# Kernel tuning notes

Hardware: AMD Instinct MI355X
Metric: run time of the kernel (lower is better)

Reference implementation:

```python
import jax, jax.numpy as jnp
import numpy as np

N = 50000      # nodes
E = 800000     # edges (avg degree 16)
IN, H, OUT = 128, 256, 2
BN_EPS = 1e-5


def setup_inputs() -> dict:
    key = jax.random.key(0)
    ks = jax.random.split(key, 24)
    w = lambda k, s: jax.random.normal(k, s, jnp.float32) * 0.05
    inp = {
        "x": jax.random.normal(ks[0], (N, IN), jnp.float32),
        "edge_index": jax.random.randint(ks[1], (2, E), 0, N, jnp.int64),
    }
    # GINConv 1 MLP: Linear(IN,H) -> BN(H) -> ReLU -> Linear(H,H) -> ReLU
    inp.update(c1_W1=w(ks[2], (IN, H)), c1_b1=w(ks[3], (H,)),
               c1_g=jnp.ones((H,), jnp.float32), c1_be=jnp.zeros((H,), jnp.float32),
               c1_W2=w(ks[4], (H, H)), c1_b2=w(ks[5], (H,)))
    # GINConv 2
    inp.update(c2_W1=w(ks[6], (H, H)), c2_b1=w(ks[7], (H,)),
               c2_g=jnp.ones((H,), jnp.float32), c2_be=jnp.zeros((H,), jnp.float32),
               c2_W2=w(ks[8], (H, H)), c2_b2=w(ks[9], (H,)))
    # GINConv 3
    inp.update(c3_W1=w(ks[10], (H, H)), c3_b1=w(ks[11], (H,)),
               c3_g=jnp.ones((H,), jnp.float32), c3_be=jnp.zeros((H,), jnp.float32),
               c3_W2=w(ks[12], (H, H)), c3_b2=w(ks[13], (H,)))
    # readout head
    inp.update(lin1_W=w(ks[14], (3 * H, 3 * H)), lin1_b=w(ks[15], (3 * H,)),
               lin2_W=w(ks[16], (3 * H, OUT)), lin2_b=w(ks[17], (OUT,)))
    return inp


def _gin_conv(x, src, dst, W1, b1, g, be, W2, b2):
    # sum-aggregate neighbor features: agg[i] = sum_{e: dst[e]==i} x[src[e]]
    agg = jax.ops.segment_sum(x[src], dst, num_segments=N)
    h = (x + agg) @ W1 + b1            # (1+eps)*x + agg, eps=0
    mu = h.mean(axis=0)
    var = h.var(axis=0)                # biased var, as torch BN training
    h = jax.nn.relu((h - mu) * jax.lax.rsqrt(var + BN_EPS) * g + be)
    return jax.nn.relu(h @ W2 + b2)


def reference(x, edge_index,
              c1_W1, c1_b1, c1_g, c1_be, c1_W2, c1_b2,
              c2_W1, c2_b1, c2_g, c2_be, c2_W2, c2_b2,
              c3_W1, c3_b1, c3_g, c3_be, c3_W2, c3_b2,
              lin1_W, lin1_b, lin2_W, lin2_b):
    src, dst = edge_index[0], edge_index[1]
    h1 = _gin_conv(x, src, dst, c1_W1, c1_b1, c1_g, c1_be, c1_W2, c1_b2)
    h2 = _gin_conv(h1, src, dst, c2_W1, c2_b1, c2_g, c2_be, c2_W2, c2_b2)
    h3 = _gin_conv(h2, src, dst, c3_W1, c3_b1, c3_g, c3_be, c3_W2, c3_b2)
    h = jnp.concatenate((h1, h2, h3), axis=1)        # [N, 3H]
    h = jax.nn.relu(h @ lin1_W + lin1_b)
    h = h @ lin2_W + lin2_b                          # [N, OUT]
    return h, jax.nn.softmax(h, axis=1)
```

## Files before the change

kernel.cpp:

```cpp
#include <hip/hip_runtime.h>
#include <hip/hip_bf16.h>


#define GIN_N_FEAT_IN 128
#define GIN_H 256
#define M_PAD_ROWS 50176

typedef short short8 __attribute__((ext_vector_type(8)));
typedef float f32x4 __attribute__((ext_vector_type(4)));

__device__ inline ushort f32_to_bf16(float f) {
    union { float f; uint u; } x; x.f = f;
    uint r = x.u + 0x7fff + ((x.u >> 16) & 1);
    return (ushort)(r >> 16);
}
__device__ inline float bf16_to_f32(uint h) {
    union { uint u; float f; } x; x.u = h << 16;
    return x.f;
}
__device__ inline uint pack_bf16(float lo, float hi) {
    return (uint)f32_to_bf16(lo) | ((uint)f32_to_bf16(hi) << 16);
}

__device__ inline void gload_lds16(const ushort* g, ushort* l) {
    __builtin_amdgcn_global_load_lds(
        (const __attribute__((address_space(1))) void*)g,
        (__attribute__((address_space(3))) void*)l, 16, 0, 0);
}


__global__ void cvt_f32_bf16(const float* __restrict__ in, ushort* __restrict__ out, int npairs) {
    for (int i = blockIdx.x * blockDim.x + threadIdx.x; i < npairs; i += gridDim.x * blockDim.x) {
        float2 v = ((const float2*)in)[i];
        ((uint*)out)[i] = pack_bf16(v.x, v.y);
    }
}

struct WPrep {
    const float* src[7];
    ushort* dst[7];
    int R[7];
    int C[7];
};

__global__ void prep_weights(WPrep p) {
    int which = blockIdx.y;
    int R = p.R[which], C = p.C[which];
    int total = R * C;
    const float* src = p.src[which];
    ushort* dst = p.dst[which];
    for (int idx = blockIdx.x * blockDim.x + threadIdx.x; idx < total;
         idx += gridDim.x * blockDim.x) {
        int r = idx / C, c = idx - r * C;
        dst[(size_t)c * R + r] = f32_to_bf16(src[idx]);
    }
}


__global__ void count_kernel(const int* __restrict__ ei, int* __restrict__ deg, int E) {
    for (int e = blockIdx.x * blockDim.x + threadIdx.x; e < E; e += gridDim.x * blockDim.x) {
        atomicAdd(&deg[ei[E + e]], 1);
    }
}

__global__ void scan_chunk(const int* __restrict__ deg, int* __restrict__ row_start,
                           int* __restrict__ chunk_sums, int N) {
    __shared__ int sm[256];
    int tid = threadIdx.x;
    int idx = blockIdx.x * 256 + tid;
    int v = (idx < N) ? deg[idx] : 0;
    sm[tid] = v;
    __syncthreads();
    #pragma unroll
    for (int off = 1; off < 256; off <<= 1) {
        int t = (tid >= off) ? sm[tid - off] : 0;
        __syncthreads();
        sm[tid] += t;
        __syncthreads();
    }
    if (idx < N) row_start[idx] = sm[tid] - v;
    if (tid == 255) chunk_sums[blockIdx.x] = sm[255];
}

__global__ void scan_tops(int* __restrict__ chunk_sums, int* __restrict__ row_start,
                          int nchunks, int N, int E) {
    __shared__ int sm[256];
    int tid = threadIdx.x;
    int v = (tid < nchunks) ? chunk_sums[tid] : 0;
    sm[tid] = v;
    __syncthreads();
    #pragma unroll
    for (int off = 1; off < 256; off <<= 1) {
        int t = (tid >= off) ? sm[tid - off] : 0;
        __syncthreads();
        sm[tid] += t;
        __syncthreads();
    }
    if (tid < nchunks) chunk_sums[tid] = sm[tid] - v;
    if (tid == 0) row_start[N] = E;
}

__global__ void scan_add(int* __restrict__ row_start, int* __restrict__ cursor,
                         const int* __restrict__ chunk_sums, int N) {
    int idx = blockIdx.x * 256 + threadIdx.x;
    if (idx < N) {
        int v = row_start[idx] + chunk_sums[blockIdx.x];
        row_start[idx] = v;
        cursor[idx] = v;
    }
}

__global__ void scatter_kernel(const int* __restrict__ ei, int* __restrict__ cursor,
                               int* __restrict__ perm, int E) {
    for (int e = blockIdx.x * blockDim.x + threadIdx.x; e < E; e += gridDim.x * blockDim.x) {
        int d = ei[E + e];
        int pos = atomicAdd(&cursor[d], 1);
        perm[pos] = ei[e];
    }
}


template <int W>
__global__ void agg2(const ushort* __restrict__ xsrc, int stride,
                     const int* __restrict__ row_start, const int* __restrict__ perm,
                     ushort* __restrict__ out, int N) {
    constexpr int PL = W / 64;
    int node = blockIdx.x * 4 + (threadIdx.x >> 6);
    if (node >= N) return;
    const int lane = threadIdx.x & 63;
    const size_t loff = (size_t)lane * PL;

    float af[PL];
    {
        const ushort* p = xsrc + (size_t)node * stride + loff;
        if constexpr (W == 256) {
            uint2 v = *(const uint2*)p;
            af[0] = bf16_to_f32(v.x & 0xffffu); af[1] = bf16_to_f32(v.x >> 16);
            af[2] = bf16_to_f32(v.y & 0xffffu); af[3] = bf16_to_f32(v.y >> 16);
        } else {
            uint v = *(const uint*)p;
            af[0] = bf16_to_f32(v & 0xffffu); af[1] = bf16_to_f32(v >> 16);
        }
    }
    const int s = row_start[node], e = row_start[node + 1];
    int j = s;
    for (; j + 4 <= e; j += 4) {
        int n0 = perm[j], n1 = perm[j + 1], n2 = perm[j + 2], n3 = perm[j + 3];
        if constexpr (W == 256) {
            uint2 w0 = *(const uint2*)(xsrc + (size_t)n0 * stride + loff);
            uint2 w1 = *(const uint2*)(xsrc + (size_t)n1 * stride + loff);
            uint2 w2 = *(const uint2*)(xsrc + (size_t)n2 * stride + loff);
            uint2 w3 = *(const uint2*)(xsrc + (size_t)n3 * stride + loff);
            af[0] += bf16_to_f32(w0.x & 0xffffu) + bf16_to_f32(w1.x & 0xffffu)
                   + bf16_to_f32(w2.x & 0xffffu) + bf16_to_f32(w3.x & 0xffffu);
            af[1] += bf16_to_f32(w0.x >> 16) + bf16_to_f32(w1.x >> 16)
                   + bf16_to_f32(w2.x >> 16) + bf16_to_f32(w3.x >> 16);
            af[2] += bf16_to_f32(w0.y & 0xffffu) + bf16_to_f32(w1.y & 0xffffu)
                   + bf16_to_f32(w2.y & 0xffffu) + bf16_to_f32(w3.y & 0xffffu);
            af[3] += bf16_to_f32(w0.y >> 16) + bf16_to_f32(w1.y >> 16)
                   + bf16_to_f32(w2.y >> 16) + bf16_to_f32(w3.y >> 16);
        } else {
            uint w0 = *(const uint*)(xsrc + (size_t)n0 * stride + loff);
            uint w1 = *(const uint*)(xsrc + (size_t)n1 * stride + loff);
            uint w2 = *(const uint*)(xsrc + (size_t)n2 * stride + loff);
            uint w3 = *(const uint*)(xsrc + (size_t)n3 * stride + loff);
            af[0] += bf16_to_f32(w0 & 0xffffu) + bf16_to_f32(w1 & 0xffffu)
                   + bf16_to_f32(w2 & 0xffffu) + bf16_to_f32(w3 & 0xffffu);
            af[1] += bf16_to_f32(w0 >> 16) + bf16_to_f32(w1 >> 16)
                   + bf16_to_f32(w2 >> 16) + bf16_to_f32(w3 >> 16);
        }
    }
    for (; j < e; ++j) {
        int sn = perm[j];
        const ushort* p = xsrc + (size_t)sn * stride + loff;
        if constexpr (W == 256) {
            uint2 w = *(const uint2*)p;
            af[0] += bf16_to_f32(w.x & 0xffffu); af[1] += bf16_to_f32(w.x >> 16);
            af[2] += bf16_to_f32(w.y & 0xffffu); af[3] += bf16_to_f32(w.y >> 16);
        } else {
            uint w = *(const uint*)p;
            af[0] += bf16_to_f32(w & 0xffffu); af[1] += bf16_to_f32(w >> 16);
        }
    }
    ushort* po = out + (size_t)node * W + loff;
    if constexpr (W == 256) {
        uint2 o; o.x = pack_bf16(af[0], af[1]); o.y = pack_bf16(af[2], af[3]);
        *(uint2*)po = o;
    } else {
        *(uint*)po = pack_bf16(af[0], af[1]);
    }
}


template <int MODE>
__global__ __launch_bounds__(256) void gemm_mfma(
    const ushort* __restrict__ A, const ushort* __restrict__ Bt,
    const float* __restrict__ bias, void* __restrict__ Cout,
    int ldc, int K, float* __restrict__ extra, int Nvalid) {
    __shared__ ushort As[128 * 32];
    __shared__ ushort Bs[128 * 32];
    const int tid = threadIdx.x;

    const int gx = gridDim.x;
    const int nwg = gx * gridDim.y;
    const int flat = blockIdx.y * gx + blockIdx.x;
    const int q = nwg >> 3, r = nwg & 7;
    const int xcd = flat & 7, loc = flat >> 3;
    const int wg = (xcd < r ? xcd * (q + 1) : r * (q + 1) + (xcd - r) * q) + loc;
    const int bm = (wg / gx) * 128;
    const int bn = (wg % gx) * 128;

    const int lane = tid & 63;
    const int wid = tid >> 6;
    const int wr = wid >> 1, wc = wid & 1;

    f32x4 acc[4][4] = {};

    const int srow = tid >> 2;
    const int skcol = (tid & 3) * 8;
    const ushort* Ag0 = A + (size_t)(bm + srow) * K + skcol;
    const ushort* Ag1 = A + (size_t)(bm + 64 + srow) * K + skcol;
    const ushort* Bg0 = Bt + (size_t)(bn + srow) * K + skcol;
    const ushort* Bg1 = Bt + (size_t)(bn + 64 + srow) * K + skcol;
    ushort* As0 = &As[(tid & ~63) * 8];
    ushort* As1 = &As[2048 + (tid & ~63) * 8];
    ushort* Bs0 = &Bs[(tid & ~63) * 8];
    ushort* Bs1 = &Bs[2048 + (tid & ~63) * 8];

    const int kk = (lane >> 4) * 8;
    const int fr = lane & 15;

    for (int k0 = 0; k0 < K; k0 += 32) {
        gload_lds16(Ag0 + k0, As0);
        gload_lds16(Ag1 + k0, As1);
        gload_lds16(Bg0 + k0, Bs0);
        gload_lds16(Bg1 + k0, Bs1);
        __syncthreads();
        short8 af[4], bf[4];
        #pragma unroll
        for (int m = 0; m < 4; ++m)
            af[m] = *(const short8*)&As[(wr * 64 + m * 16 + fr) * 32 + kk];
        #pragma unroll
        for (int n = 0; n < 4; ++n)
            bf[n] = *(const short8*)&Bs[(wc * 64 + n * 16 + fr) * 32 + kk];
        #pragma unroll
        for (int m = 0; m < 4; ++m)
            #pragma unroll
            for (int n = 0; n < 4; ++n)
                acc[m][n] = __builtin_amdgcn_mfma_f32_16x16x32_bf16(af[m], bf[n], acc[m][n], 0, 0, 0);
        __syncthreads();
    }

    float s1[4], s2[4];
    if constexpr (MODE == 0) {
        #pragma unroll
        for (int n = 0; n < 4; ++n) { s1[n] = 0.f; s2[n] = 0.f; }
    }
    #pragma unroll
    for (int n = 0; n < 4; ++n) {
        const int col = bn + wc * 64 + n * 16 + fr;
        const float bv = bias[col];
        #pragma unroll
        for (int m = 0; m < 4; ++m) {
            const int row0 = bm + wr * 64 + m * 16 + (lane >> 4) * 4;
            #pragma unroll
            for (int rr = 0; rr < 4; ++rr) {
                float v = acc[m][n][rr] + bv;
                if constexpr (MODE == 1) {
                    v = fmaxf(v, 0.f);
                    ((ushort*)Cout)[(size_t)(row0 + rr) * ldc + col] = f32_to_bf16(v);
                } else {
                    ((float*)Cout)[(size_t)(row0 + rr) * ldc + col] = v;
                    if (row0 + rr < Nvalid) { s1[n] += v; s2[n] += v * v; }
                }
            }
        }
    }
    if constexpr (MODE == 0) {
        #pragma unroll
        for (int n = 0; n < 4; ++n) {
            float a = s1[n], b = s2[n];
            a += __shfl_xor(a, 16); b += __shfl_xor(b, 16);
            a += __shfl_xor(a, 32); b += __shfl_xor(b, 32);
            if ((lane >> 4) == 0) {
                int col = bn + wc * 64 + n * 16 + fr;
                atomicAdd(&extra[col], a);
                atomicAdd(&extra[256 + col], b);
            }
        }
    }
}


__global__ __launch_bounds__(512) void gemm_head(
    const ushort* __restrict__ A,
    const ushort* __restrict__ Bt,
    const float* __restrict__ bias,
    const float* __restrict__ w2,
    float* __restrict__ part,
    int K, int MP) {
    __shared__ ushort As[256 * 64];
    __shared__ ushort Bs[128 * 64];
    __shared__ float sm_part[256][2];
    const int tid = threadIdx.x;

    const int gx = gridDim.x;
    const int nwg = gx * gridDim.y;
    const int flat = blockIdx.y * gx + blockIdx.x;
    const int q = nwg >> 3, r = nwg & 7;
    const int xcd = flat & 7, loc = flat >> 3;
    const int wg = (xcd < r ? xcd * (q + 1) : r * (q + 1) + (xcd - r) * q) + loc;
    const int bm = (wg / gx) * 256;
    const int bn = (wg % gx) * 128;
    const int coltile = wg % gx;

    const int lane = tid & 63;
    const int wid = tid >> 6;
    const int wr = wid >> 1;
    const int wc = wid & 1;

    sm_part[tid >> 1][tid & 1] = 0.f;

    f32x4 acc[4][4] = {};

    const int grow = tid >> 3;
    const int gcol = (tid & 7) * 8;
    const int wbase = (tid & ~63) * 8;
    const int kko = (lane >> 4) * 8;
    const int fr = lane & 15;

    for (int k0 = 0; k0 < K; k0 += 64) {
        #pragma unroll
        for (int c = 0; c < 4; ++c)
            gload_lds16(A + (size_t)(bm + c * 64 + grow) * K + k0 + gcol,
                        &As[c * 4096 + wbase]);
        #pragma unroll
        for (int c = 0; c < 2; ++c)
            gload_lds16(Bt + (size_t)(bn + c * 64 + grow) * K + k0 + gcol,
                        &Bs[c * 4096 + wbase]);
        __syncthreads();
        #pragma unroll
        for (int ksub = 0; ksub < 2; ++ksub) {
            short8 af[4], bf[4];
            #pragma unroll
            for (int m = 0; m < 4; ++m)
                af[m] = *(const short8*)&As[(wr * 64 + m * 16 + fr) * 64 + ksub * 32 + kko];
            #pragma unroll
            for (int n = 0; n < 4; ++n)
                bf[n] = *(const short8*)&Bs[(wc * 64 + n * 16 + fr) * 64 + ksub * 32 + kko];
            #pragma unroll
            for (int m = 0; m < 4; ++m)
                #pragma unroll
                for (int n = 0; n < 4; ++n)
                    acc[m][n] = __builtin_amdgcn_mfma_f32_16x16x32_bf16(af[m], bf[n], acc[m][n], 0, 0, 0);
        }
        __syncthreads();
    }

    #pragma unroll
    for (int m = 0; m < 4; ++m) {
        #pragma unroll
        for (int rr = 0; rr < 4; ++rr) {
            float o0 = 0.f, o1 = 0.f;
            #pragma unroll
            for (int n = 0; n < 4; ++n) {
                int col = bn + wc * 64 + n * 16 + fr;
                float v = fmaxf(acc[m][n][rr] + bias[col], 0.f);
                o0 = fmaf(v, w2[col * 2 + 0], o0);
                o1 = fmaf(v, w2[col * 2 + 1], o1);
            }
            o0 += __shfl_xor(o0, 1); o1 += __shfl_xor(o1, 1);
            o0 += __shfl_xor(o0, 2); o1 += __shfl_xor(o1, 2);
            o0 += __shfl_xor(o0, 4); o1 += __shfl_xor(o1, 4);
            o0 += __shfl_xor(o0, 8); o1 += __shfl_xor(o1, 8);
            if (fr == 0) {
                int lrow = wr * 64 + m * 16 + (lane >> 4) * 4 + rr;
                atomicAdd(&sm_part[lrow][0], o0);
                atomicAdd(&sm_part[lrow][1], o1);
            }
        }
    }
    __syncthreads();
    {
        int lrow = tid >> 1, comp = tid & 1;
        part[((size_t)coltile * MP + bm + lrow) * 2 + comp] = sm_part[lrow][comp];
    }
}


__global__ void bn_apply(const float* __restrict__ h, const float* __restrict__ sums,
                         const float* __restrict__ g, const float* __restrict__ be,
                         ushort* __restrict__ outb, int Nrows) {
    int total = Nrows * 128;
    float inv = 1.0f / (float)Nrows;
    for (int idx = blockIdx.x * blockDim.x + threadIdx.x; idx < total;
         idx += gridDim.x * blockDim.x) {
        int row = idx >> 7;
        int cp = (idx & 127) * 2;
        float2 v = *(const float2*)(h + (size_t)row * 256 + cp);
        float mu0 = sums[cp] * inv,     mu1 = sums[cp + 1] * inv;
        float va0 = sums[256 + cp] * inv - mu0 * mu0;
        float va1 = sums[257 + cp] * inv - mu1 * mu1;
        float o0 = fmaxf((v.x - mu0) * rsqrtf(va0 + 1e-5f) * g[cp]     + be[cp],     0.f);
        float o1 = fmaxf((v.y - mu1) * rsqrtf(va1 + 1e-5f) * g[cp + 1] + be[cp + 1], 0.f);
        *(uint*)(outb + (size_t)row * 256 + cp) = pack_bf16(o0, o1);
    }
}


__global__ void finalize6(const float* __restrict__ part, const float* __restrict__ b2,
                          float* __restrict__ out, int Nrows, int MP) {
    int i = blockIdx.x * blockDim.x + threadIdx.x;
    if (i >= Nrows) return;
    float h0 = b2[0], h1 = b2[1];
    #pragma unroll
    for (int c = 0; c < 6; ++c) {
        h0 += part[((size_t)c * MP + i) * 2 + 0];
        h1 += part[((size_t)c * MP + i) * 2 + 1];
    }
    out[2 * i] = h0;
    out[2 * i + 1] = h1;
    float m = fmaxf(h0, h1);
    float e0 = expf(h0 - m), e1 = expf(h1 - m);
    float s = e0 + e1;
    out[(size_t)2 * Nrows + 2 * i] = e0 / s;
    out[(size_t)2 * Nrows + 2 * i + 1] = e1 / s;
}


extern "C" void kernel_launch(void* const* d_in, const int* in_sizes, int n_in,
                              void* d_out, int out_size, void* d_ws, size_t ws_size,
                              hipStream_t stream) {
    const int N = in_sizes[0] / GIN_N_FEAT_IN;
    const int E = in_sizes[1] / 2;
    const int MP = M_PAD_ROWS;
    const int nchunks = (N + 255) / 256;

    const float* x  = (const float*)d_in[0];
    const int*   ei = (const int*)d_in[1];
    const float* cW1[3] = {(const float*)d_in[2],  (const float*)d_in[8],  (const float*)d_in[14]};
    const float* cb1[3] = {(const float*)d_in[3],  (const float*)d_in[9],  (const float*)d_in[15]};
    const float* cg [3] = {(const float*)d_in[4],  (const float*)d_in[10], (const float*)d_in[16]};
    const float* cbe[3] = {(const float*)d_in[5],  (const float*)d_in[11], (const float*)d_in[17]};
    const float* cW2[3] = {(const float*)d_in[6],  (const float*)d_in[12], (const float*)d_in[18]};
    const float* cb2[3] = {(const float*)d_in[7],  (const float*)d_in[13], (const float*)d_in[19]};
    const float* lin1_W = (const float*)d_in[20];
    const float* lin1_b = (const float*)d_in[21];
    const float* lin2_W = (const float*)d_in[22];
    const float* lin2_b = (const float*)d_in[23];
    float* out = (float*)d_out;

    char* ws = (char*)d_ws;
    size_t off = 0;
    auto carve = [&](size_t bytes) {
        void* p = ws + off;
        off += (bytes + 255) & ~(size_t)255;
        return p;
    };
    ushort* Hcat   = (ushort*)carve((size_t)MP * 768 * 2);
    float*  hlin   = (float*) carve((size_t)MP * 256 * 4);
    ushort* hlin_b = (ushort*)carve((size_t)MP * 256 * 2);
    ushort* hpre   = (ushort*)carve((size_t)MP * 256 * 2);
    ushort* xb     = (ushort*)carve((size_t)MP * 128 * 2);
    ushort* w1t[3] = {(ushort*)carve(256 * 256 * 2), (ushort*)carve(256 * 256 * 2),
                      (ushort*)carve(256 * 256 * 2)};
    ushort* w2t[3] = {(ushort*)carve(256 * 256 * 2), (ushort*)carve(256 * 256 * 2),
                      (ushort*)carve(256 * 256 * 2)};
    ushort* lin1t  = (ushort*)carve((size_t)768 * 768 * 2);
    int*   row_st  = (int*)carve((size_t)(N + 1) * 4);
    int*   cursor  = (int*)carve((size_t)N * 4);
    int*   perm    = (int*)carve((size_t)E * 4);
    int*   csums   = (int*)carve(256 * 4);
    float* bnsums  = (float*)carve(512 * 4);
    float* part    = (float*)carve((size_t)6 * MP * 2 * 4);
    (void)ws_size;

    cvt_f32_bf16<<<1024, 256, 0, stream>>>(x, xb, N * 64);
    WPrep wp;
    wp.src[0] = cW1[0]; wp.dst[0] = w1t[0]; wp.R[0] = 128; wp.C[0] = 256;
    wp.src[1] = cW1[1]; wp.dst[1] = w1t[1]; wp.R[1] = 256; wp.C[1] = 256;
    wp.src[2] = cW1[2]; wp.dst[2] = w1t[2]; wp.R[2] = 256; wp.C[2] = 256;
    wp.src[3] = cW2[0]; wp.dst[3] = w2t[0]; wp.R[3] = 256; wp.C[3] = 256;
    wp.src[4] = cW2[1]; wp.dst[4] = w2t[1]; wp.R[4] = 256; wp.C[4] = 256;
    wp.src[5] = cW2[2]; wp.dst[5] = w2t[2]; wp.R[5] = 256; wp.C[5] = 256;
    wp.src[6] = lin1_W; wp.dst[6] = lin1t;  wp.R[6] = 768; wp.C[6] = 768;
    prep_weights<<<dim3(576, 7), 256, 0, stream>>>(wp);

    hipMemsetAsync(cursor, 0, (size_t)N * 4, stream);
    count_kernel<<<1024, 256, 0, stream>>>(ei, cursor, E);
    scan_chunk<<<nchunks, 256, 0, stream>>>(cursor, row_st, csums, N);
    scan_tops<<<1, 256, 0, stream>>>(csums, row_st, nchunks, N, E);
    scan_add<<<nchunks, 256, 0, stream>>>(row_st, cursor, csums, N);
    scatter_kernel<<<1024, 256, 0, stream>>>(ei, cursor, perm, E);

    const dim3 ggrid(2, MP / 128);
    const int aggblocks = (N + 3) / 4;

    for (int L = 0; L < 3; ++L) {
        if (L == 0)
            agg2<128><<<aggblocks, 256, 0, stream>>>(xb, 128, row_st, perm, hpre, N);
        else
            agg2<256><<<aggblocks, 256, 0, stream>>>(Hcat + (size_t)(L - 1) * 256, 768,
                                                     row_st, perm, hpre, N);

        hipMemsetAsync(bnsums, 0, 512 * 4, stream);
        gemm_mfma<0><<<ggrid, 256, 0, stream>>>(
            hpre, w1t[L], cb1[L], hlin, 256, (L == 0) ? 128 : 256, bnsums, N);

        bn_apply<<<2048, 256, 0, stream>>>(hlin, bnsums, cg[L], cbe[L], hlin_b, N);

        gemm_mfma<1><<<ggrid, 256, 0, stream>>>(
            hlin_b, w2t[L], cb2[L], (void*)(Hcat + (size_t)L * 256), 768, 256,
            nullptr, 0);
    }

    gemm_head<<<dim3(6, MP / 256), 512, 0, stream>>>(
        Hcat, lin1t, lin1_b, lin2_W, part, 768, MP);

    finalize6<<<(N + 255) / 256, 256, 0, stream>>>(part, lin2_b, out, N, MP);
}
```

Measured before the change: 686.9 us.

## Double-buffer LDS tiles and XOR-swizzle chunks in both MFMA GEMM kernels

Both GEMM kernels now keep two LDS buffers and issue the global-to-LDS loads for the next K-tile before computing on the current one. This overlaps memory latency with MFMA work and removes one barrier per iteration. The 16-byte K-chunks are also XOR-swizzled by row on store and read back with a matching swizzle, to reduce LDS bank conflicts. The head kernel's K-step drops from 64 to 32, so it needs more iterations, and LDS use changes slightly.

```diff
diff --git a/kernel.cpp b/kernel.cpp
--- a/kernel.cpp
+++ b/kernel.cpp
@@ -197,8 +197,8 @@
     const ushort* __restrict__ A, const ushort* __restrict__ Bt,
     const float* __restrict__ bias, void* __restrict__ Cout,
     int ldc, int K, float* __restrict__ extra, int Nvalid) {
-    __shared__ ushort As[128 * 32];
-    __shared__ ushort Bs[128 * 32];
+    __shared__ ushort As[2][128 * 32];
+    __shared__ ushort Bs[2][128 * 32];
     const int tid = threadIdx.x;
 
     const int gx = gridDim.x;
@@ -216,33 +216,46 @@
 
     f32x4 acc[4][4] = {};
 
-    const int srow = tid >> 2;
-    const int skcol = (tid & 3) * 8;
-    const ushort* Ag0 = A + (size_t)(bm + srow) * K + skcol;
-    const ushort* Ag1 = A + (size_t)(bm + 64 + srow) * K + skcol;
-    const ushort* Bg0 = Bt + (size_t)(bn + srow) * K + skcol;
-    const ushort* Bg1 = Bt + (size_t)(bn + 64 + srow) * K + skcol;
-    ushort* As0 = &As[(tid & ~63) * 8];
-    ushort* As1 = &As[2048 + (tid & ~63) * 8];
-    ushort* Bs0 = &Bs[(tid & ~63) * 8];
-    ushort* Bs1 = &Bs[2048 + (tid & ~63) * 8];
-
-    const int kk = (lane >> 4) * 8;
+    const int arow = tid >> 2;
+    const int gcol = ((tid & 3) ^ ((tid >> 3) & 3)) * 8;
+    const ushort* Ag0 = A + (size_t)(bm + arow) * K + gcol;
+    const ushort* Ag1 = A + (size_t)(bm + 64 + arow) * K + gcol;
+    const ushort* Bg0 = Bt + (size_t)(bn + arow) * K + gcol;
+    const ushort* Bg1 = Bt + (size_t)(bn + 64 + arow) * K + gcol;
+    const int wofs = (tid & ~63) * 8;
+
     const int fr = lane & 15;
-
-    for (int k0 = 0; k0 < K; k0 += 32) {
-        gload_lds16(Ag0 + k0, As0);
-        gload_lds16(Ag1 + k0, As1);
-        gload_lds16(Bg0 + k0, Bs0);
-        gload_lds16(Bg1 + k0, Bs1);
-        __syncthreads();
+    const int rchunk = ((lane >> 4) ^ ((fr >> 1) & 3)) * 8;
+
+    const int NT = K >> 5;
+
+    {
+        ushort* a = As[0]; ushort* b = Bs[0];
+        gload_lds16(Ag0, a + wofs);
+        gload_lds16(Ag1, a + 2048 + wofs);
+        gload_lds16(Bg0, b + wofs);
+        gload_lds16(Bg1, b + 2048 + wofs);
+    }
+    __syncthreads();
+
+    for (int it = 0; it < NT; ++it) {
+        if (it + 1 < NT) {
+            const int k0 = (it + 1) << 5;
+            ushort* a = As[(it + 1) & 1]; ushort* b = Bs[(it + 1) & 1];
+            gload_lds16(Ag0 + k0, a + wofs);
+            gload_lds16(Ag1 + k0, a + 2048 + wofs);
+            gload_lds16(Bg0 + k0, b + wofs);
+            gload_lds16(Bg1 + k0, b + 2048 + wofs);
+        }
+        const ushort* as = As[it & 1];
+        const ushort* bs = Bs[it & 1];
         short8 af[4], bf[4];
         #pragma unroll
         for (int m = 0; m < 4; ++m)
-            af[m] = *(const short8*)&As[(wr * 64 + m * 16 + fr) * 32 + kk];
+            af[m] = *(const short8*)&as[(wr * 64 + m * 16 + fr) * 32 + rchunk];
         #pragma unroll
         for (int n = 0; n < 4; ++n)
-            bf[n] = *(const short8*)&Bs[(wc * 64 + n * 16 + fr) * 32 + kk];
+            bf[n] = *(const short8*)&bs[(wc * 64 + n * 16 + fr) * 32 + rchunk];
         #pragma unroll
         for (int m = 0; m < 4; ++m)
             #pragma unroll
@@ -299,8 +312,8 @@
     const float* __restrict__ w2,
     float* __restrict__ part,
     int K, int MP) {
-    __shared__ ushort As[256 * 64];
-    __shared__ ushort Bs[128 * 64];
+    __shared__ ushort As[2][256 * 32];
+    __shared__ ushort Bs[2][128 * 32];
     __shared__ float sm_part[256][2];
     const int tid = threadIdx.x;
 
@@ -323,37 +336,48 @@
 
     f32x4 acc[4][4] = {};
 
-    const int grow = tid >> 3;
-    const int gcol = (tid & 7) * 8;
-    const int wbase = (tid & ~63) * 8;
-    const int kko = (lane >> 4) * 8;
+    const int arow = tid >> 2;
+    const int gcol = ((tid & 3) ^ ((tid >> 3) & 3)) * 8;
+    const ushort* Ag0 = A + (size_t)(bm + arow) * K + gcol;
+    const ushort* Ag1 = A + (size_t)(bm + 128 + arow) * K + gcol;
+    const ushort* Bg0 = Bt + (size_t)(bn + arow) * K + gcol;
+    const int wofs = (tid & ~63) * 8;
+
     const int fr = lane & 15;
-
-    for (int k0 = 0; k0 < K; k0 += 64) {
-        #pragma unroll
-        for (int c = 0; c < 4; ++c)
-            gload_lds16(A + (size_t)(bm + c * 64 + grow) * K + k0 + gcol,
-                        &As[c * 4096 + wbase]);
-        #pragma unroll
-        for (int c = 0; c < 2; ++c)
-            gload_lds16(Bt + (size_t)(bn + c * 64 + grow) * K + k0 + gcol,
-                        &Bs[c * 4096 + wbase]);
-        __syncthreads();
-        #pragma unroll
-        for (int ksub = 0; ksub < 2; ++ksub) {
-            short8 af[4], bf[4];
-            #pragma unroll
-            for (int m = 0; m < 4; ++m)
-                af[m] = *(const short8*)&As[(wr * 64 + m * 16 + fr) * 64 + ksub * 32 + kko];
+    const int rchunk = ((lane >> 4) ^ ((fr >> 1) & 3)) * 8;
+
+    const int NT = K >> 5;
+
+    {
+        ushort* a = As[0]; ushort* b = Bs[0];
+        gload_lds16(Ag0, a + wofs);
+        gload_lds16(Ag1, a + 4096 + wofs);
+        gload_lds16(Bg0, b + wofs);
+    }
+    __syncthreads();
+
+    for (int it = 0; it < NT; ++it) {
+        if (it + 1 < NT) {
+            const int k0 = (it + 1) << 5;
+            ushort* a = As[(it + 1) & 1]; ushort* b = Bs[(it + 1) & 1];
+            gload_lds16(Ag0 + k0, a + wofs);
+            gload_lds16(Ag1 + k0, a + 4096 + wofs);
+            gload_lds16(Bg0 + k0, b + wofs);
+        }
+        const ushort* as = As[it & 1];
+        const ushort* bs = Bs[it & 1];
+        short8 af[4], bf[4];
+        #pragma unroll
+        for (int m = 0; m < 4; ++m)
+            af[m] = *(const short8*)&as[(wr * 64 + m * 16 + fr) * 32 + rchunk];
+        #pragma unroll
+        for (int n = 0; n < 4; ++n)
+            bf[n] = *(const short8*)&bs[(wc * 64 + n * 16 + fr) * 32 + rchunk];
+        #pragma unroll
+        for (int m = 0; m < 4; ++m)
             #pragma unroll
             for (int n = 0; n < 4; ++n)
-                bf[n] = *(const short8*)&Bs[(wc * 64 + n * 16 + fr) * 64 + ksub * 32 + kko];
-            #pragma unroll
-            for (int m = 0; m < 4; ++m)
-                #pragma unroll
-                for (int n = 0; n < 4; ++n)
-                    acc[m][n] = __builtin_amdgcn_mfma_f32_16x16x32_bf16(af[m], bf[n], acc[m][n], 0, 0, 0);
-        }
+                acc[m][n] = __builtin_amdgcn_mfma_f32_16x16x32_bf16(af[m], bf[n], acc[m][n], 0, 0, 0);
         __syncthreads();
     }
 
```

New measurement: 677.1 us. No clear change (-1.4%).
